# Kernel tuning notes

Measured on AMD Instinct MI355X. Metric: run time of the kernel, lower is better.

The kernel has to match this reference:

```python
import jax, jax.numpy as jnp
import numpy as np

B, S, C, H = 256, 512, 512, 512
MOG_ITERS = 5


def _xavier(key, shape):
    fan_out, fan_in = shape
    lim = float(np.sqrt(6.0 / (fan_in + fan_out)))
    return jax.random.uniform(key, shape, minval=-lim, maxval=lim, dtype=jnp.float32)


def setup_inputs() -> dict:
    key = jax.random.key(0)
    ks = jax.random.split(key, 7)
    x = jax.random.normal(ks[0], (B, S, C), dtype=jnp.float32)
    return {
        "x": x,
        "Wih_w": _xavier(ks[1], (4 * H, C)), "Wih_b": jnp.zeros((4 * H,), jnp.float32),
        "Wmx_w": _xavier(ks[2], (H, C)),     "Wmx_b": jnp.zeros((H,), jnp.float32),
        "Wmh_w": _xavier(ks[3], (H, H)),     "Wmh_b": jnp.zeros((H,), jnp.float32),
        "Whm_w": _xavier(ks[4], (4 * H, H)), "Whm_b": jnp.zeros((4 * H,), jnp.float32),
        "Q": _xavier(ks[5], (H, C)),
        "R": _xavier(ks[6], (C, H)),
    }


def _mogrify(xt, ht, Q, R):
    # alternating mogrifier rounds; odd i updates xt, even i updates ht
    for i in range(1, MOG_ITERS + 1):
        if i % 2 == 1:
            xt = 2.0 * jax.nn.sigmoid(ht @ Q) * xt  # (B,H)@(H,C) -> (B,C)
        else:
            ht = 2.0 * jax.nn.sigmoid(xt @ R) * ht  # (B,C)@(C,H) -> (B,H)
    return xt, ht


def reference(x, Wih_w, Wih_b, Wmx_w, Wmx_b, Wmh_w, Wmh_b, Whm_w, Whm_b, Q, R):
    batch = x.shape[0]
    h0 = jnp.zeros((batch, H), x.dtype)
    c0 = jnp.zeros((batch, H), x.dtype)

    def step(carry, xt):
        ht, Ct = carry
        xt, ht = _mogrify(xt, ht, Q, R)
        mt = xt @ Wmx_w.T + Wmx_b + ht @ Wmh_w.T + Wmh_b          # (B,H)
        gates = xt @ Wih_w.T + Wih_b + mt @ Whm_w.T + Whm_b        # (B,4H)
        i_g, f_g, g_g, o_g = jnp.split(gates, 4, axis=1)
        Ct = jax.nn.sigmoid(f_g) * Ct + jax.nn.sigmoid(i_g) * jnp.tanh(g_g)
        ht = jax.nn.sigmoid(o_g) * jnp.tanh(Ct)
        return (ht, Ct), ht

    xs = jnp.swapaxes(x, 0, 1)                  # (S,B,C)
    _, hs = jax.lax.scan(step, (h0, c0), xs)    # (S,B,H)
    return jnp.swapaxes(hs, 0, 1)               # (B,S,H)
```

## Files before the change

kernel.cpp:

```cpp
#include <hip/hip_runtime.h>
#include <hip/hip_bf16.h>

#define Bdim 256
#define Sdim 512
#define Cdim 512
#define Hdim 512

typedef __attribute__((ext_vector_type(8))) short bfrag;
typedef __attribute__((ext_vector_type(8))) unsigned short u16x8;
typedef __attribute__((ext_vector_type(4))) float f32x4;

__device__ __forceinline__ unsigned short f2bf_rne(float f) {
    union { float f; unsigned u; } v; v.f = f;
    return (unsigned short)((v.u + 0x7fffu + ((v.u >> 16) & 1u)) >> 16);
}
__device__ __forceinline__ float sigmoidf_(float x) { return 1.0f / (1.0f + __expf(-x)); }

template<bool TRANS>
__global__ __launch_bounds__(256) void pack_weight(const float* __restrict__ src,
                                                   unsigned short* __restrict__ dst,
                                                   int K, int N) {
    int tid = blockIdx.x * 256 + threadIdx.x;
    int total = (K >> 5) * (N >> 4) * 64;
    if (tid >= total) return;
    int lane = tid & 63;
    int blk  = tid >> 6;
    int kc   = blk & 15;
    int n16  = blk >> 4;
    int n  = (n16 << 4) + (lane & 15);
    int kb = (kc << 5) + ((lane >> 4) << 3);
    u16x8 v;
#pragma unroll
    for (int j = 0; j < 8; ++j) {
        int k = kb + j;
        float f = TRANS ? src[(size_t)n * K + k] : src[(size_t)k * N + n];
        v[j] = f2bf_rne(f);
    }
    *(u16x8*)(dst + ((size_t)tid << 3)) = v;
}

__global__ __launch_bounds__(256) void zero_state(float* hf, float* cs, unsigned short* hb) {
    int tid = blockIdx.x * 256 + threadIdx.x;
    if (tid < Bdim * Hdim) { hf[tid] = 0.f; cs[tid] = 0.f; hb[tid] = 0; }
}

__global__ __launch_bounds__(64)
void mog_kernel(const unsigned short* __restrict__ A,
                const unsigned short* __restrict__ Wp,
                const float* __restrict__ prev, long prevStride,
                float* __restrict__ dstf, unsigned short* __restrict__ dstb)
{
    int nt = blockIdx.x, mt = blockIdx.y;
    int lane = threadIdx.x, lm = lane & 15, lq = lane >> 4;
    f32x4 acc[2][2] = {};
    const bfrag* A0 = (const bfrag*)(A + (size_t)(mt*32 +      lm) * 512) + lq;
    const bfrag* A1 = (const bfrag*)(A + (size_t)(mt*32 + 16 + lm) * 512) + lq;
    const bfrag* B0 = (const bfrag*)(Wp + (size_t)(nt*2    ) * 16 * 512) + lane;
    const bfrag* B1 = (const bfrag*)(Wp + (size_t)(nt*2 + 1) * 16 * 512) + lane;
#pragma unroll 4
    for (int kc = 0; kc < 16; ++kc) {
        bfrag a0 = A0[kc*4], a1 = A1[kc*4];
        bfrag b0 = B0[kc*64], b1 = B1[kc*64];
        acc[0][0] = __builtin_amdgcn_mfma_f32_16x16x32_bf16(a0, b0, acc[0][0], 0, 0, 0);
        acc[0][1] = __builtin_amdgcn_mfma_f32_16x16x32_bf16(a0, b1, acc[0][1], 0, 0, 0);
        acc[1][0] = __builtin_amdgcn_mfma_f32_16x16x32_bf16(a1, b0, acc[1][0], 0, 0, 0);
        acc[1][1] = __builtin_amdgcn_mfma_f32_16x16x32_bf16(a1, b1, acc[1][1], 0, 0, 0);
    }
    int nb = nt*32, mb = mt*32;
#pragma unroll
    for (int mi = 0; mi < 2; ++mi)
#pragma unroll
    for (int ni = 0; ni < 2; ++ni) {
        int n = nb + ni*16 + lm;
#pragma unroll
        for (int r = 0; r < 4; ++r) {
            int m = mb + mi*16 + lq*4 + r;
            float g = 2.0f * sigmoidf_(acc[mi][ni][r]);
            float v = g * prev[(size_t)m * prevStride + n];
            dstf[(size_t)m * 512 + n] = v;
            dstb[(size_t)m * 512 + n] = f2bf_rne(v);
        }
    }
}

__global__ __launch_bounds__(64)
void mt_kernel(const unsigned short* __restrict__ X,
               const unsigned short* __restrict__ Hm,
               const unsigned short* __restrict__ W1p,
               const unsigned short* __restrict__ W2p,
               const float* __restrict__ b1, const float* __restrict__ b2,
               unsigned short* __restrict__ mtb)
{
    int nt = blockIdx.x, mt = blockIdx.y;
    int lane = threadIdx.x, lm = lane & 15, lq = lane >> 4;
    f32x4 acc[2][2] = {};
    const unsigned short* As[2] = {X, Hm};
    const unsigned short* Ws[2] = {W1p, W2p};
#pragma unroll
    for (int ph = 0; ph < 2; ++ph) {
        const bfrag* A0 = (const bfrag*)(As[ph] + (size_t)(mt*32 +      lm) * 512) + lq;
        const bfrag* A1 = (const bfrag*)(As[ph] + (size_t)(mt*32 + 16 + lm) * 512) + lq;
        const bfrag* B0 = (const bfrag*)(Ws[ph] + (size_t)(nt*2    ) * 16 * 512) + lane;
        const bfrag* B1 = (const bfrag*)(Ws[ph] + (size_t)(nt*2 + 1) * 16 * 512) + lane;
#pragma unroll 4
        for (int kc = 0; kc < 16; ++kc) {
            bfrag a0 = A0[kc*4], a1 = A1[kc*4];
            bfrag b0 = B0[kc*64], b1 = B1[kc*64];
            acc[0][0] = __builtin_amdgcn_mfma_f32_16x16x32_bf16(a0, b0, acc[0][0], 0, 0, 0);
            acc[0][1] = __builtin_amdgcn_mfma_f32_16x16x32_bf16(a0, b1, acc[0][1], 0, 0, 0);
            acc[1][0] = __builtin_amdgcn_mfma_f32_16x16x32_bf16(a1, b0, acc[1][0], 0, 0, 0);
            acc[1][1] = __builtin_amdgcn_mfma_f32_16x16x32_bf16(a1, b1, acc[1][1], 0, 0, 0);
        }
    }
    int nb = nt*32, mb = mt*32;
#pragma unroll
    for (int mi = 0; mi < 2; ++mi)
#pragma unroll
    for (int ni = 0; ni < 2; ++ni) {
        int n = nb + ni*16 + lm;
        float bias = b1[n] + b2[n];
#pragma unroll
        for (int r = 0; r < 4; ++r) {
            int m = mb + mi*16 + lq*4 + r;
            mtb[(size_t)m * 512 + n] = f2bf_rne(acc[mi][ni][r] + bias);
        }
    }
}

__global__ __launch_bounds__(64)
void gates_cell_kernel(const unsigned short* __restrict__ X,
                       const unsigned short* __restrict__ Mt,
                       const unsigned short* __restrict__ Wihp,
                       const unsigned short* __restrict__ Whmp,
                       const float* __restrict__ bih, const float* __restrict__ bhm,
                       float* __restrict__ Cs, float* __restrict__ hf,
                       unsigned short* __restrict__ hb,
                       float* __restrict__ outp )
{
    int nt = blockIdx.x, mt = blockIdx.y;
    int lane = threadIdx.x, lm = lane & 15, lq = lane >> 4;
    f32x4 acc[4][2][2] = {};
    const unsigned short* As[2] = {X, Mt};
    const unsigned short* Ws[2] = {Wihp, Whmp};
#pragma unroll
    for (int ph = 0; ph < 2; ++ph) {
        const bfrag* A0 = (const bfrag*)(As[ph] + (size_t)(mt*32 +      lm) * 512) + lq;
        const bfrag* A1 = (const bfrag*)(As[ph] + (size_t)(mt*32 + 16 + lm) * 512) + lq;
        const unsigned short* W = Ws[ph];
#pragma unroll 2
        for (int kc = 0; kc < 16; ++kc) {
            bfrag a0 = A0[kc*4], a1 = A1[kc*4];
#pragma unroll
            for (int g = 0; g < 4; ++g) {
                const bfrag* B0 = (const bfrag*)(W + ((size_t)(g*32 + nt*2) * 16 + kc) * 512) + lane;
                bfrag b0 = B0[0];
                bfrag b1 = B0[1024];
                acc[g][0][0] = __builtin_amdgcn_mfma_f32_16x16x32_bf16(a0, b0, acc[g][0][0], 0, 0, 0);
                acc[g][0][1] = __builtin_amdgcn_mfma_f32_16x16x32_bf16(a0, b1, acc[g][0][1], 0, 0, 0);
                acc[g][1][0] = __builtin_amdgcn_mfma_f32_16x16x32_bf16(a1, b0, acc[g][1][0], 0, 0, 0);
                acc[g][1][1] = __builtin_amdgcn_mfma_f32_16x16x32_bf16(a1, b1, acc[g][1][1], 0, 0, 0);
            }
        }
    }
    int nb = nt*32, mb = mt*32;
#pragma unroll
    for (int mi = 0; mi < 2; ++mi)
#pragma unroll
    for (int ni = 0; ni < 2; ++ni) {
        int n = nb + ni*16 + lm;
        float bi = bih[n]        + bhm[n];
        float bf = bih[512 + n]  + bhm[512 + n];
        float bg = bih[1024 + n] + bhm[1024 + n];
        float bo = bih[1536 + n] + bhm[1536 + n];
#pragma unroll
        for (int r = 0; r < 4; ++r) {
            int m = mb + mi*16 + lq*4 + r;
            size_t idx = (size_t)m * 512 + n;
            float ig = sigmoidf_(acc[0][mi][ni][r] + bi);
            float fg = sigmoidf_(acc[1][mi][ni][r] + bf);
            float gg = tanhf    (acc[2][mi][ni][r] + bg);
            float og = sigmoidf_(acc[3][mi][ni][r] + bo);
            float c  = fg * Cs[idx] + ig * gg;
            Cs[idx] = c;
            float h = og * tanhf(c);
            hf[idx] = h;
            hb[idx] = f2bf_rne(h);
            outp[(size_t)m * (Sdim * Hdim) + n] = h;
        }
    }
}

extern "C" void kernel_launch(void* const* d_in, const int* in_sizes, int n_in,
                              void* d_out, int out_size, void* d_ws, size_t ws_size,
                              hipStream_t stream) {
    const float* x     = (const float*)d_in[0];
    const float* Wih_w = (const float*)d_in[1];
    const float* Wih_b = (const float*)d_in[2];
    const float* Wmx_w = (const float*)d_in[3];
    const float* Wmx_b = (const float*)d_in[4];
    const float* Wmh_w = (const float*)d_in[5];
    const float* Wmh_b = (const float*)d_in[6];
    const float* Whm_w = (const float*)d_in[7];
    const float* Whm_b = (const float*)d_in[8];
    const float* Q     = (const float*)d_in[9];
    const float* R     = (const float*)d_in[10];
    float* out = (float*)d_out;

    unsigned short* packQ   = (unsigned short*)d_ws;
    unsigned short* packR   = packQ   + 512 * 512;
    unsigned short* packWmx = packR   + 512 * 512;
    unsigned short* packWmh = packWmx + 512 * 512;
    unsigned short* packWih = packWmh + 512 * 512;
    unsigned short* packWhm = packWih + 512 * 2048;
    float* xtf = (float*)(packWhm + 512 * 2048);
    float* hf  = xtf + Bdim * Cdim;
    float* cs  = hf  + Bdim * Hdim;
    unsigned short* xtb = (unsigned short*)(cs + Bdim * Hdim);
    unsigned short* hb  = xtb + Bdim * Cdim;
    unsigned short* mtb = hb  + Bdim * Hdim;

    pack_weight<false><<<dim3(128), dim3(256), 0, stream>>>(Q,     packQ,   512, 512);
    pack_weight<false><<<dim3(128), dim3(256), 0, stream>>>(R,     packR,   512, 512);
    pack_weight<true ><<<dim3(128), dim3(256), 0, stream>>>(Wmx_w, packWmx, 512, 512);
    pack_weight<true ><<<dim3(128), dim3(256), 0, stream>>>(Wmh_w, packWmh, 512, 512);
    pack_weight<true ><<<dim3(512), dim3(256), 0, stream>>>(Wih_w, packWih, 512, 2048);
    pack_weight<true ><<<dim3(512), dim3(256), 0, stream>>>(Whm_w, packWhm, 512, 2048);
    zero_state<<<dim3(512), dim3(256), 0, stream>>>(hf, cs, hb);

    dim3 grid(16, 8), block(64);
    for (int t = 0; t < Sdim; ++t) {
        const float* xsrc = x + (size_t)t * Cdim;
        mog_kernel<<<grid, block, 0, stream>>>(hb,  packQ, xsrc, (long)(Sdim * Cdim), xtf, xtb);
        mog_kernel<<<grid, block, 0, stream>>>(xtb, packR, hf,   512, hf,  hb);
        mog_kernel<<<grid, block, 0, stream>>>(hb,  packQ, xtf,  512, xtf, xtb);
        mog_kernel<<<grid, block, 0, stream>>>(xtb, packR, hf,   512, hf,  hb);
        mog_kernel<<<grid, block, 0, stream>>>(hb,  packQ, xtf,  512, xtf, xtb);
        mt_kernel<<<grid, block, 0, stream>>>(xtb, hb, packWmx, packWmh, Wmx_b, Wmh_b, mtb);
        gates_cell_kernel<<<grid, block, 0, stream>>>(xtb, mtb, packWih, packWhm,
                                                      Wih_b, Whm_b, cs, hf, hb,
                                                      out + (size_t)t * Hdim);
    }
}
```

Baseline: 35.04 ms.

## Fold weight chain into one matrix and run a persistent kernel with group barriers

Precomputes combined weights W' = [Wmx^T Whm^T + Wih^T ; Wmh^T Whm^T] and a folded bias, so each step needs a single K=1024 GEMM for the gates instead of the mt GEMM followed by the gates GEMM. Replaces the seven per-timestep launches (over 3500 kernel launches in total) with one persistent kernel of 128 workgroups. Each group of 16 workgroups owns 32 batch rows and synchronises through atomic-counter barriers. This removes launch overhead and one GEMM stage per step. It changes bf16 rounding, since the folded product is rounded once, and relies on all 128 workgroups being co-resident for the spin barriers.

```diff
diff --git a/kernel.cpp b/kernel.cpp
--- a/kernel.cpp
+++ b/kernel.cpp
@@ -16,13 +16,9 @@
 }
 __device__ __forceinline__ float sigmoidf_(float x) { return 1.0f / (1.0f + __expf(-x)); }
 
-template<bool TRANS>
 __global__ __launch_bounds__(256) void pack_weight(const float* __restrict__ src,
-                                                   unsigned short* __restrict__ dst,
-                                                   int K, int N) {
+                                                   unsigned short* __restrict__ dst) {
     int tid = blockIdx.x * 256 + threadIdx.x;
-    int total = (K >> 5) * (N >> 4) * 64;
-    if (tid >= total) return;
     int lane = tid & 63;
     int blk  = tid >> 6;
     int kc   = blk & 15;
@@ -31,162 +27,181 @@
     int kb = (kc << 5) + ((lane >> 4) << 3);
     u16x8 v;
 #pragma unroll
-    for (int j = 0; j < 8; ++j) {
-        int k = kb + j;
-        float f = TRANS ? src[(size_t)n * K + k] : src[(size_t)k * N + n];
-        v[j] = f2bf_rne(f);
+    for (int j = 0; j < 8; ++j) v[j] = f2bf_rne(src[(size_t)(kb + j) * 512 + n]);
+    *(u16x8*)(dst + ((size_t)tid << 3)) = v;
+}
+
+__global__ __launch_bounds__(256) void build_wcat(const float* __restrict__ Wmx,
+                                                  const float* __restrict__ Wmh,
+                                                  const float* __restrict__ Whm,
+                                                  const float* __restrict__ Wih,
+                                                  unsigned short* __restrict__ packW) {
+    __shared__ float As[16][17], Bs[16][17];
+    int kk0 = blockIdx.x * 16, o0 = blockIdx.y * 16;
+    int tl = threadIdx.x & 15, th = threadIdx.x >> 4;
+    int kk = kk0 + th;
+    float acc = 0.f;
+    for (int j0 = 0; j0 < 512; j0 += 16) {
+        As[th][tl] = (kk < 512) ? Wmx[(size_t)(j0 + tl) * 512 + kk]
+                                : Wmh[(size_t)(j0 + tl) * 512 + (kk - 512)];
+        Bs[th][tl] = Whm[(size_t)(o0 + th) * 512 + j0 + tl];
+        __syncthreads();
+#pragma unroll
+        for (int j = 0; j < 16; ++j) acc += As[th][j] * Bs[tl][j];
+        __syncthreads();
     }
-    *(u16x8*)(dst + ((size_t)tid << 3)) = v;
-}
-
-__global__ __launch_bounds__(256) void zero_state(float* hf, float* cs, unsigned short* hb) {
+    int o = o0 + tl;
+    if (kk < 512) acc += Wih[(size_t)o * 512 + kk];
+    int gi = o >> 9, n = o & 511;
+    int cp = (n >> 5) * 128 + gi * 32 + (n & 31);
+    int n16 = cp >> 4, kc = kk >> 5, r = kk & 31;
+    int lane = ((r >> 3) << 4) | (cp & 15), j = r & 7;
+    packW[((size_t)(n16 * 32 + kc) << 9) + lane * 8 + j] = f2bf_rne(acc);
+}
+
+__global__ __launch_bounds__(256) void build_bias(const float* __restrict__ Wmx_b,
+                                                  const float* __restrict__ Wmh_b,
+                                                  const float* __restrict__ Whm,
+                                                  const float* __restrict__ Wih_b,
+                                                  const float* __restrict__ Whm_b,
+                                                  float* __restrict__ bprime) {
+    int o = blockIdx.x * 256 + threadIdx.x;
+    if (o >= 2048) return;
+    float s = 0.f;
+    for (int j = 0; j < 512; ++j) s += (Wmx_b[j] + Wmh_b[j]) * Whm[(size_t)o * 512 + j];
+    bprime[o] = s + Wih_b[o] + Whm_b[o];
+}
+
+__global__ __launch_bounds__(256) void init_state(float* hm, float* cm,
+                                                  unsigned short* axh, unsigned* bars) {
     int tid = blockIdx.x * 256 + threadIdx.x;
-    if (tid < Bdim * Hdim) { hf[tid] = 0.f; cs[tid] = 0.f; hb[tid] = 0; }
-}
-
-__global__ __launch_bounds__(64)
-void mog_kernel(const unsigned short* __restrict__ A,
-                const unsigned short* __restrict__ Wp,
-                const float* __restrict__ prev, long prevStride,
-                float* __restrict__ dstf, unsigned short* __restrict__ dstb)
-{
-    int nt = blockIdx.x, mt = blockIdx.y;
-    int lane = threadIdx.x, lm = lane & 15, lq = lane >> 4;
-    f32x4 acc[2][2] = {};
-    const bfrag* A0 = (const bfrag*)(A + (size_t)(mt*32 +      lm) * 512) + lq;
-    const bfrag* A1 = (const bfrag*)(A + (size_t)(mt*32 + 16 + lm) * 512) + lq;
-    const bfrag* B0 = (const bfrag*)(Wp + (size_t)(nt*2    ) * 16 * 512) + lane;
-    const bfrag* B1 = (const bfrag*)(Wp + (size_t)(nt*2 + 1) * 16 * 512) + lane;
-#pragma unroll 4
-    for (int kc = 0; kc < 16; ++kc) {
-        bfrag a0 = A0[kc*4], a1 = A1[kc*4];
-        bfrag b0 = B0[kc*64], b1 = B1[kc*64];
-        acc[0][0] = __builtin_amdgcn_mfma_f32_16x16x32_bf16(a0, b0, acc[0][0], 0, 0, 0);
-        acc[0][1] = __builtin_amdgcn_mfma_f32_16x16x32_bf16(a0, b1, acc[0][1], 0, 0, 0);
-        acc[1][0] = __builtin_amdgcn_mfma_f32_16x16x32_bf16(a1, b0, acc[1][0], 0, 0, 0);
-        acc[1][1] = __builtin_amdgcn_mfma_f32_16x16x32_bf16(a1, b1, acc[1][1], 0, 0, 0);
+    if (tid < Bdim * Hdim) {
+        hm[tid] = 0.f; cm[tid] = 0.f;
+        int m = tid >> 9, n = tid & 511;
+        axh[(size_t)m * 1024 + 512 + n] = 0;
     }
-    int nb = nt*32, mb = mt*32;
-#pragma unroll
-    for (int mi = 0; mi < 2; ++mi)
-#pragma unroll
-    for (int ni = 0; ni < 2; ++ni) {
-        int n = nb + ni*16 + lm;
-#pragma unroll
-        for (int r = 0; r < 4; ++r) {
-            int m = mb + mi*16 + lq*4 + r;
-            float g = 2.0f * sigmoidf_(acc[mi][ni][r]);
-            float v = g * prev[(size_t)m * prevStride + n];
-            dstf[(size_t)m * 512 + n] = v;
-            dstb[(size_t)m * 512 + n] = f2bf_rne(v);
-        }
-    }
-}
-
-__global__ __launch_bounds__(64)
-void mt_kernel(const unsigned short* __restrict__ X,
-               const unsigned short* __restrict__ Hm,
-               const unsigned short* __restrict__ W1p,
-               const unsigned short* __restrict__ W2p,
-               const float* __restrict__ b1, const float* __restrict__ b2,
-               unsigned short* __restrict__ mtb)
-{
-    int nt = blockIdx.x, mt = blockIdx.y;
-    int lane = threadIdx.x, lm = lane & 15, lq = lane >> 4;
-    f32x4 acc[2][2] = {};
-    const unsigned short* As[2] = {X, Hm};
-    const unsigned short* Ws[2] = {W1p, W2p};
-#pragma unroll
-    for (int ph = 0; ph < 2; ++ph) {
-        const bfrag* A0 = (const bfrag*)(As[ph] + (size_t)(mt*32 +      lm) * 512) + lq;
-        const bfrag* A1 = (const bfrag*)(As[ph] + (size_t)(mt*32 + 16 + lm) * 512) + lq;
-        const bfrag* B0 = (const bfrag*)(Ws[ph] + (size_t)(nt*2    ) * 16 * 512) + lane;
-        const bfrag* B1 = (const bfrag*)(Ws[ph] + (size_t)(nt*2 + 1) * 16 * 512) + lane;
+    if (tid < 8 * 64) bars[tid] = 0;
+}
+
+__global__ __launch_bounds__(256, 2)
+void moglstm_persist(const float* __restrict__ xin,
+                     const unsigned short* __restrict__ packQ,
+                     const unsigned short* __restrict__ packR,
+                     const unsigned short* __restrict__ packW,
+                     const float* __restrict__ bprime,
+                     unsigned short* __restrict__ axh,
+                     float* __restrict__ xm, float* __restrict__ hm,
+                     float* __restrict__ cm,
+                     unsigned* __restrict__ bars,
+                     float* __restrict__ out) {
+    __shared__ float gacc[4 * 32 * 33];
+    const int wg  = blockIdx.x;
+    const int grp = wg >> 4, wgi = wg & 15;
+    const int tid  = threadIdx.x;
+    const int lane = tid & 63, wv = tid >> 6;
+    const int lm = lane & 15, lq = lane >> 4;
+    const int mb = grp * 32;
+    volatile unsigned* cnt = bars + grp * 64;
+    unsigned nbar = 0;
+
+    auto barrier = [&]() {
+        __syncthreads();
+        if (tid == 0) {
+            __threadfence();
+            atomicAdd((unsigned*)cnt, 1u);
+            ++nbar;
+            unsigned target = nbar * 16u;
+            while (*cnt < target) __builtin_amdgcn_s_sleep(2);
+            __threadfence();
+        }
+        __syncthreads();
+    };
+
+    auto mog = [&](unsigned short* buf, int apart, const unsigned short* pack,
+                   const float* prev, size_t prevStride, int dpart, float* dstf) {
+        const int rh = wv & 1, ch = wv >> 1;
+        const int arow = mb + rh * 16 + lm;
+        const bfrag* A = (const bfrag*)(buf + (size_t)arow * 1024 + apart);
+        const unsigned short* Bbase = pack + ((size_t)(wgi * 2 + ch) << 13);
+        f32x4 acc = {};
 #pragma unroll 4
         for (int kc = 0; kc < 16; ++kc) {
-            bfrag a0 = A0[kc*4], a1 = A1[kc*4];
-            bfrag b0 = B0[kc*64], b1 = B1[kc*64];
-            acc[0][0] = __builtin_amdgcn_mfma_f32_16x16x32_bf16(a0, b0, acc[0][0], 0, 0, 0);
-            acc[0][1] = __builtin_amdgcn_mfma_f32_16x16x32_bf16(a0, b1, acc[0][1], 0, 0, 0);
-            acc[1][0] = __builtin_amdgcn_mfma_f32_16x16x32_bf16(a1, b0, acc[1][0], 0, 0, 0);
-            acc[1][1] = __builtin_amdgcn_mfma_f32_16x16x32_bf16(a1, b1, acc[1][1], 0, 0, 0);
-        }
-    }
-    int nb = nt*32, mb = mt*32;
-#pragma unroll
-    for (int mi = 0; mi < 2; ++mi)
-#pragma unroll
-    for (int ni = 0; ni < 2; ++ni) {
-        int n = nb + ni*16 + lm;
-        float bias = b1[n] + b2[n];
+            bfrag a = A[kc * 4 + lq];
+            bfrag b = *((const bfrag*)(Bbase + ((size_t)kc << 9)) + lane);
+            acc = __builtin_amdgcn_mfma_f32_16x16x32_bf16(a, b, acc, 0, 0, 0);
+        }
+        const int n = wgi * 32 + ch * 16 + lm;
 #pragma unroll
         for (int r = 0; r < 4; ++r) {
-            int m = mb + mi*16 + lq*4 + r;
-            mtb[(size_t)m * 512 + n] = f2bf_rne(acc[mi][ni][r] + bias);
-        }
-    }
-}
-
-__global__ __launch_bounds__(64)
-void gates_cell_kernel(const unsigned short* __restrict__ X,
-                       const unsigned short* __restrict__ Mt,
-                       const unsigned short* __restrict__ Wihp,
-                       const unsigned short* __restrict__ Whmp,
-                       const float* __restrict__ bih, const float* __restrict__ bhm,
-                       float* __restrict__ Cs, float* __restrict__ hf,
-                       unsigned short* __restrict__ hb,
-                       float* __restrict__ outp )
-{
-    int nt = blockIdx.x, mt = blockIdx.y;
-    int lane = threadIdx.x, lm = lane & 15, lq = lane >> 4;
-    f32x4 acc[4][2][2] = {};
-    const unsigned short* As[2] = {X, Mt};
-    const unsigned short* Ws[2] = {Wihp, Whmp};
-#pragma unroll
-    for (int ph = 0; ph < 2; ++ph) {
-        const bfrag* A0 = (const bfrag*)(As[ph] + (size_t)(mt*32 +      lm) * 512) + lq;
-        const bfrag* A1 = (const bfrag*)(As[ph] + (size_t)(mt*32 + 16 + lm) * 512) + lq;
-        const unsigned short* W = Ws[ph];
+            int m = mb + rh * 16 + lq * 4 + r;
+            float v = 2.f * sigmoidf_(acc[r]) * prev[(size_t)m * prevStride + n];
+            dstf[(size_t)m * 512 + n] = v;
+            buf[(size_t)m * 1024 + dpart + n] = f2bf_rne(v);
+        }
+    };
+
+    for (int t = 0; t < Sdim; ++t) {
+        unsigned short* cur = axh + (size_t)(t & 1) * (256 * 1024);
+        unsigned short* nxt = axh + (size_t)((t + 1) & 1) * (256 * 1024);
+
+        mog(cur, 512, packQ, xin + (size_t)t * 512, (size_t)Sdim * 512, 0, xm);
+        barrier();
+        mog(cur, 0, packR, hm, 512, 512, hm);
+        barrier();
+        mog(cur, 512, packQ, xm, 512, 0, xm);
+        barrier();
+        mog(cur, 0, packR, hm, 512, 512, hm);
+        barrier();
+        mog(cur, 512, packQ, xm, 512, 0, xm);
+        barrier();
+
+        {
+            const int n16b = wgi * 8 + wv * 2;
+            f32x4 acc[2][2] = {};
+            const bfrag* A0 = (const bfrag*)(cur + (size_t)(mb + lm) * 1024);
+            const bfrag* A1 = (const bfrag*)(cur + (size_t)(mb + 16 + lm) * 1024);
 #pragma unroll 2
-        for (int kc = 0; kc < 16; ++kc) {
-            bfrag a0 = A0[kc*4], a1 = A1[kc*4];
-#pragma unroll
-            for (int g = 0; g < 4; ++g) {
-                const bfrag* B0 = (const bfrag*)(W + ((size_t)(g*32 + nt*2) * 16 + kc) * 512) + lane;
-                bfrag b0 = B0[0];
-                bfrag b1 = B0[1024];
-                acc[g][0][0] = __builtin_amdgcn_mfma_f32_16x16x32_bf16(a0, b0, acc[g][0][0], 0, 0, 0);
-                acc[g][0][1] = __builtin_amdgcn_mfma_f32_16x16x32_bf16(a0, b1, acc[g][0][1], 0, 0, 0);
-                acc[g][1][0] = __builtin_amdgcn_mfma_f32_16x16x32_bf16(a1, b0, acc[g][1][0], 0, 0, 0);
-                acc[g][1][1] = __builtin_amdgcn_mfma_f32_16x16x32_bf16(a1, b1, acc[g][1][1], 0, 0, 0);
+            for (int kc = 0; kc < 32; ++kc) {
+                bfrag a0 = A0[kc * 4 + lq], a1 = A1[kc * 4 + lq];
+                bfrag b0 = *((const bfrag*)(packW + ((size_t)(n16b * 32 + kc) << 9)) + lane);
+                bfrag b1 = *((const bfrag*)(packW + ((size_t)((n16b + 1) * 32 + kc) << 9)) + lane);
+                acc[0][0] = __builtin_amdgcn_mfma_f32_16x16x32_bf16(a0, b0, acc[0][0], 0, 0, 0);
+                acc[0][1] = __builtin_amdgcn_mfma_f32_16x16x32_bf16(a0, b1, acc[0][1], 0, 0, 0);
+                acc[1][0] = __builtin_amdgcn_mfma_f32_16x16x32_bf16(a1, b0, acc[1][0], 0, 0, 0);
+                acc[1][1] = __builtin_amdgcn_mfma_f32_16x16x32_bf16(a1, b1, acc[1][1], 0, 0, 0);
             }
-        }
-    }
-    int nb = nt*32, mb = mt*32;
-#pragma unroll
-    for (int mi = 0; mi < 2; ++mi)
-#pragma unroll
-    for (int ni = 0; ni < 2; ++ni) {
-        int n = nb + ni*16 + lm;
-        float bi = bih[n]        + bhm[n];
-        float bf = bih[512 + n]  + bhm[512 + n];
-        float bg = bih[1024 + n] + bhm[1024 + n];
-        float bo = bih[1536 + n] + bhm[1536 + n];
-#pragma unroll
-        for (int r = 0; r < 4; ++r) {
-            int m = mb + mi*16 + lq*4 + r;
-            size_t idx = (size_t)m * 512 + n;
-            float ig = sigmoidf_(acc[0][mi][ni][r] + bi);
-            float fg = sigmoidf_(acc[1][mi][ni][r] + bf);
-            float gg = tanhf    (acc[2][mi][ni][r] + bg);
-            float og = sigmoidf_(acc[3][mi][ni][r] + bo);
-            float c  = fg * Cs[idx] + ig * gg;
-            Cs[idx] = c;
-            float h = og * tanhf(c);
-            hf[idx] = h;
-            hb[idx] = f2bf_rne(h);
-            outp[(size_t)m * (Sdim * Hdim) + n] = h;
-        }
+#pragma unroll
+            for (int mi = 0; mi < 2; ++mi)
+#pragma unroll
+            for (int ni = 0; ni < 2; ++ni) {
+                int nn = ni * 16 + lm;
+                float bias = bprime[wv * 512 + wgi * 32 + nn];
+#pragma unroll
+                for (int r = 0; r < 4; ++r) {
+                    int mrow = mi * 16 + lq * 4 + r;
+                    gacc[(wv * 32 + mrow) * 33 + nn] = acc[mi][ni][r] + bias;
+                }
+            }
+            __syncthreads();
+            int ncol = lane & 31, rb = lane >> 5;
+#pragma unroll
+            for (int rr = 0; rr < 4; ++rr) {
+                int mrow = wv * 8 + rb * 4 + rr;
+                float ig = gacc[(0 * 32 + mrow) * 33 + ncol];
+                float fg = gacc[(1 * 32 + mrow) * 33 + ncol];
+                float gg = gacc[(2 * 32 + mrow) * 33 + ncol];
+                float og = gacc[(3 * 32 + mrow) * 33 + ncol];
+                int m = mb + mrow, n = wgi * 32 + ncol;
+                size_t idx = (size_t)m * 512 + n;
+                float c = sigmoidf_(fg) * cm[idx] + sigmoidf_(ig) * tanhf(gg);
+                cm[idx] = c;
+                float h = sigmoidf_(og) * tanhf(c);
+                hm[idx] = h;
+                nxt[(size_t)m * 1024 + 512 + n] = f2bf_rne(h);
+                out[((size_t)m * 512 + t) * 512 + n] = h;
+            }
+        }
+        barrier();
     }
 }
 
@@ -206,38 +221,22 @@
     const float* R     = (const float*)d_in[10];
     float* out = (float*)d_out;
 
-    unsigned short* packQ   = (unsigned short*)d_ws;
-    unsigned short* packR   = packQ   + 512 * 512;
-    unsigned short* packWmx = packR   + 512 * 512;
-    unsigned short* packWmh = packWmx + 512 * 512;
-    unsigned short* packWih = packWmh + 512 * 512;
-    unsigned short* packWhm = packWih + 512 * 2048;
-    float* xtf = (float*)(packWhm + 512 * 2048);
-    float* hf  = xtf + Bdim * Cdim;
-    float* cs  = hf  + Bdim * Hdim;
-    unsigned short* xtb = (unsigned short*)(cs + Bdim * Hdim);
-    unsigned short* hb  = xtb + Bdim * Cdim;
-    unsigned short* mtb = hb  + Bdim * Hdim;
-
-    pack_weight<false><<<dim3(128), dim3(256), 0, stream>>>(Q,     packQ,   512, 512);
-    pack_weight<false><<<dim3(128), dim3(256), 0, stream>>>(R,     packR,   512, 512);
-    pack_weight<true ><<<dim3(128), dim3(256), 0, stream>>>(Wmx_w, packWmx, 512, 512);
-    pack_weight<true ><<<dim3(128), dim3(256), 0, stream>>>(Wmh_w, packWmh, 512, 512);
-    pack_weight<true ><<<dim3(512), dim3(256), 0, stream>>>(Wih_w, packWih, 512, 2048);
-    pack_weight<true ><<<dim3(512), dim3(256), 0, stream>>>(Whm_w, packWhm, 512, 2048);
-    zero_state<<<dim3(512), dim3(256), 0, stream>>>(hf, cs, hb);
-
-    dim3 grid(16, 8), block(64);
-    for (int t = 0; t < Sdim; ++t) {
-        const float* xsrc = x + (size_t)t * Cdim;
-        mog_kernel<<<grid, block, 0, stream>>>(hb,  packQ, xsrc, (long)(Sdim * Cdim), xtf, xtb);
-        mog_kernel<<<grid, block, 0, stream>>>(xtb, packR, hf,   512, hf,  hb);
-        mog_kernel<<<grid, block, 0, stream>>>(hb,  packQ, xtf,  512, xtf, xtb);
-        mog_kernel<<<grid, block, 0, stream>>>(xtb, packR, hf,   512, hf,  hb);
-        mog_kernel<<<grid, block, 0, stream>>>(hb,  packQ, xtf,  512, xtf, xtb);
-        mt_kernel<<<grid, block, 0, stream>>>(xtb, hb, packWmx, packWmh, Wmx_b, Wmh_b, mtb);
-        gates_cell_kernel<<<grid, block, 0, stream>>>(xtb, mtb, packWih, packWhm,
-                                                      Wih_b, Whm_b, cs, hf, hb,
-                                                      out + (size_t)t * Hdim);
-    }
-}
+    unsigned short* packQ = (unsigned short*)d_ws;
+    unsigned short* packR = packQ + 512 * 512;
+    unsigned short* packW = packR + 512 * 512;
+    float* bprime = (float*)(packW + 1024 * 2048);
+    unsigned short* axh = (unsigned short*)(bprime + 2048);
+    float* xm = (float*)(axh + 2 * 256 * 1024);
+    float* hm = xm + Bdim * Cdim;
+    float* cm = hm + Bdim * Hdim;
+    unsigned* bars = (unsigned*)(cm + Bdim * Hdim);
+
+    pack_weight<<<dim3(128), dim3(256), 0, stream>>>(Q, packQ);
+    pack_weight<<<dim3(128), dim3(256), 0, stream>>>(R, packR);
+    build_wcat<<<dim3(64, 128), dim3(256), 0, stream>>>(Wmx_w, Wmh_w, Whm_w, Wih_w, packW);
+    build_bias<<<dim3(8), dim3(256), 0, stream>>>(Wmx_b, Wmh_b, Whm_w, Wih_b, Whm_b, bprime);
+    init_state<<<dim3(512), dim3(256), 0, stream>>>(hm, cm, axh, bars);
+
+    moglstm_persist<<<dim3(128), dim3(256), 0, stream>>>(
+        x, packQ, packR, packW, bprime, axh, xm, hm, cm, bars, out);
+}
```

Result: slower. 38.62 ms (+10.2%).
